# Kernel optimization log

Measured on AMD Instinct MI355X. Metric: run time of the kernel, lower is better.

Reference implementation:

```python
import jax, jax.numpy as jnp
import numpy as np

D = 768      # hidden_dim
H = 12       # num_heads
DH = D // H  # head_dim = 64
L = 12       # num_layers
V = 50257    # vocab_size
M = 16       # mini_batch_size (TTT chunk)
LR = 1.0     # ttt_learning_rate
EPS = 1e-5
ROPE_BASE = 10000.0


def _ln(x, w, b):
    mu = jnp.mean(x, axis=-1, keepdims=True)
    var = jnp.mean((x - mu) ** 2, axis=-1, keepdims=True)
    return (x - mu) / jnp.sqrt(var + EPS) * w + b


def _rope(x):
    # x: (B, H, S, DH)
    S, dh = x.shape[2], x.shape[3]
    half = dh // 2
    freqs = 1.0 / (ROPE_BASE ** (jnp.arange(half, dtype=x.dtype) / half))
    ang = jnp.arange(S, dtype=x.dtype)[:, None] * freqs[None, :]  # (S, half)
    cos, sin = jnp.cos(ang), jnp.sin(ang)
    x1, x2 = x[..., :half], x[..., half:]
    return jnp.concatenate([x1 * cos - x2 * sin, x1 * sin + x2 * cos], axis=-1)


def setup_inputs() -> dict:
    key = jax.random.key(0)
    ks = jax.random.split(key, 12)
    std = 0.02
    B, S = 4, 1024
    inp = {
        "input_ids": jax.random.randint(ks[0], (B, S), 0, V),
        "tok_emb": jax.random.normal(ks[1], (V, D), jnp.float32) * std,
        "emb_ln_w": jnp.ones((D,), jnp.float32),
        "emb_ln_b": jnp.zeros((D,), jnp.float32),
        "wq": jax.random.normal(ks[2], (L, D, D), jnp.float32) * std,
        "wk": jax.random.normal(ks[3], (L, D, D), jnp.float32) * std,
        "wv": jax.random.normal(ks[4], (L, D, D), jnp.float32) * std,
        "wo": jax.random.normal(ks[5], (L, D, D), jnp.float32) * std,
        "n1w": jnp.ones((L, D), jnp.float32),
        "n1b": jnp.zeros((L, D), jnp.float32),
        "n2w": jnp.ones((L, D), jnp.float32),
        "n2b": jnp.zeros((L, D), jnp.float32),
        "m1w": jax.random.normal(ks[6], (L, D, 4 * D), jnp.float32) * std,
        "m1b": jnp.zeros((L, 4 * D), jnp.float32),
        "m2w": jax.random.normal(ks[7], (L, 4 * D, D), jnp.float32) * std,
        "m2b": jnp.zeros((L, D), jnp.float32),
        "onw": jnp.ones((D,), jnp.float32),
        "onb": jnp.zeros((D,), jnp.float32),
    }
    return inp


def _forward(input_ids, tok_emb, emb_ln_w, emb_ln_b, wq, wk, wv, wo,
             n1w, n1b, n2w, n2b, m1w, m1b, m2w, m2b, onw, onb):
    B, S = input_ids.shape
    nc = S // M
    eta = LR / M
    mask = jnp.tril(jnp.ones((M, M), tok_emb.dtype))

    x = tok_emb[input_ids]                      # (B, S, D) token embedding
    x = _ln(x, emb_ln_w, emb_ln_b)

    def layer(x, p):
        (lwq, lwk, lwv, lwo, ln1w, ln1b, ln2w, ln2b,
         lm1w, lm1b, lm2w, lm2b) = p
        h = _ln(x, ln1w, ln1b)

        def proj(w):
            return (h @ w).reshape(B, S, H, DH).transpose(0, 2, 1, 3)  # (B,H,S,DH)

        q, k, v = proj(lwq), proj(lwk), proj(lwv)
        q, k = _rope(q), _rope(k)

        def chunks(t):  # (B,H,S,DH) -> (nc,B,H,M,DH)
            return t.reshape(B, H, nc, M, DH).transpose(2, 0, 1, 3, 4)

        qc, kc, vc = chunks(q), chunks(k), chunks(v)
        W0 = jnp.zeros((B, H, DH, DH), x.dtype)  # fast-weight state per head

        def step(W, c):
            qm, km, vm = c                                   # (B,H,M,DH)
            # reconstruction error of current fast weights on this chunk
            E = jnp.einsum('bhmd,bhde->bhme', km, W) - vm    # (B,H,M,DH)
            # causal intra-chunk correction (dual form of per-token GD)
            A = jnp.einsum('bhmd,bhnd->bhmn', qm, km) * mask
            O = (jnp.einsum('bhmd,bhde->bhme', qm, W)
                 - eta * jnp.einsum('bhmn,bhne->bhme', A, E))
            Wn = W - eta * jnp.einsum('bhmd,bhme->bhde', km, E)
            return Wn, O

        _, O = jax.lax.scan(step, W0, (qc, kc, vc))          # (nc,B,H,M,DH)
        o = O.transpose(1, 2, 0, 3, 4).reshape(B, H, S, DH)
        o = o.transpose(0, 2, 1, 3).reshape(B, S, D)
        x = x + o @ lwo

        h2 = _ln(x, ln2w, ln2b)
        x = x + jax.nn.gelu(h2 @ lm1w + lm1b) @ lm2w + lm2b
        return x, None

    x, _ = jax.lax.scan(layer, x,
                        (wq, wk, wv, wo, n1w, n1b, n2w, n2b,
                         m1w, m1b, m2w, m2b))
    x = _ln(x, onw, onb)
    logits = x @ tok_emb.T                                    # tied LM head
    return logits


def reference(input_ids, tok_emb, emb_ln_w, emb_ln_b, wq, wk, wv, wo,
              n1w, n1b, n2w, n2b, m1w, m1b, m2w, m2b, onw, onb):
    return _forward(input_ids, tok_emb, emb_ln_w, emb_ln_b, wq, wk, wv, wo,
                    n1w, n1b, n2w, n2b, m1w, m1b, m2w, m2b, onw, onb)
```

## Files before the change

### kernel.cpp

```cpp
#include <hip/hip_runtime.h>
#include <cstdint>
#include <cstddef>

#define Dm 768
#define Hh 12
#define DHd 64
#define Ll 12
#define Vv 50257
#define Vp 50304
#define Tt 4096
#define Ff 3072
#define QS 2304
#define ETA (1.0f/16.0f)

typedef __attribute__((ext_vector_type(8))) _Float16 half8;
typedef __attribute__((ext_vector_type(8))) unsigned short ushort8;
typedef __attribute__((ext_vector_type(4))) float f32x4;

static __device__ __forceinline__ unsigned short f2h(float f){
  union { _Float16 h; unsigned short u; } c; c.h = (_Float16)f; return c.u;
}
static __device__ __forceinline__ float h2f(unsigned short u){
  union { unsigned short u; _Float16 h; } c; c.u = u; return (float)c.h;
}
static __device__ __forceinline__ float4 h4(ushort4 u){
  float4 f; f.x=h2f(u.x); f.y=h2f(u.y); f.z=h2f(u.z); f.w=h2f(u.w); return f;
}
static __device__ __forceinline__ void gload16(const void* g, void* l){
  __builtin_amdgcn_global_load_lds((const __attribute__((address_space(1))) unsigned int*)g,
                                   (__attribute__((address_space(3))) unsigned int*)l, 16, 0, 0);
}
static __device__ __forceinline__ size_t pan_off(int ks, size_t M, int row, int k){
  return ((size_t)ks*M + row)*128 + (size_t)(((k*2) ^ ((row & 7) << 4)));
}

__global__ __launch_bounds__(256)
void convwt_kernel(const float* __restrict__ src, unsigned short* __restrict__ dst,
                   int K, int Ns, int Nd, int coff)
{
  const int l  = blockIdx.y;
  const int nb = blockIdx.x % (Ns/64);
  const int ks = blockIdx.x / (Ns/64);
  const int t  = threadIdx.x;
  __shared__ float tile[64][65];
  const float* W = src + (size_t)l*K*Ns;
  {
    const int r = t >> 2, c0 = (t & 3) * 16;
    const float* s = W + (size_t)(ks*64 + r)*Ns + nb*64 + c0;
    #pragma unroll
    for (int i = 0; i < 4; ++i) {
      const float4 f = *(const float4*)(s + i*4);
      tile[r][c0+i*4+0]=f.x; tile[r][c0+i*4+1]=f.y; tile[r][c0+i*4+2]=f.z; tile[r][c0+i*4+3]=f.w;
    }
  }
  __syncthreads();
  const int n   = t >> 2;
  const int kk0 = (t & 3) * 16;
  const int gn  = coff + nb*64 + n;
  unsigned short bh[16];
  #pragma unroll
  for (int i = 0; i < 16; ++i) bh[i] = f2h(tile[kk0 + i][n]);
  const size_t rowb = ((size_t)l*K*Nd + ((size_t)ks*Nd + gn)*64) * 2;
  const int swz = (gn & 7) << 4;
  char* bD = (char*)dst + rowb;
  *(ushort8*)(bD + ((kk0*2)      ^ swz)) = *(ushort8*)&bh[0];
  *(ushort8*)(bD + ((kk0*2 + 16) ^ swz)) = *(ushort8*)&bh[8];
}

__global__ __launch_bounds__(256)
void convtok_kernel(const float* __restrict__ src, unsigned short* __restrict__ dst)
{
  const int total = 12 * Vp * 8;
  for (int gi = blockIdx.x*256 + threadIdx.x; gi < total; gi += gridDim.x*256) {
    const int j  = gi & 7;
    const int v  = (gi >> 3) % Vp;
    const int ks = gi / (8 * Vp);
    ushort8 u;
    if (v < Vv) {
      const float* s = src + (size_t)v*Dm + ks*64 + j*8;
      const float4 f0 = *(const float4*)s, f1 = *(const float4*)(s+4);
      u[0]=f2h(f0.x); u[1]=f2h(f0.y); u[2]=f2h(f0.z); u[3]=f2h(f0.w);
      u[4]=f2h(f1.x); u[5]=f2h(f1.y); u[6]=f2h(f1.z); u[7]=f2h(f1.w);
    } else {
      #pragma unroll
      for (int q = 0; q < 8; ++q) u[q] = 0;
    }
    const size_t rowb = ((size_t)ks*Vp + v) * 128;
    *(ushort8*)((char*)dst + rowb + ((j*16) ^ ((v&7)<<4))) = u;
  }
}

__global__ __launch_bounds__(256)
void rtab_kernel(float* __restrict__ rt)
{
  const int idx = blockIdx.x*256 + threadIdx.x;
  if (idx >= 1024*64) return;
  const int s = idx >> 6, c = idx & 63, d = c & 31;
  const float freq = powf(10000.0f, -(float)d * (1.0f/32.0f));
  const float ang  = (float)s * freq;
  rt[idx] = (c < 32) ? cosf(ang) : sinf(ang);
}

template<int OMODE>
__global__ __launch_bounds__(256)
void ln_kernel(const float* __restrict__ in, const int* __restrict__ ids,
               const float* __restrict__ w, const float* __restrict__ b,
               void* __restrict__ o1)
{
  const int row = blockIdx.x;
  const int t = threadIdx.x;
  const float* px = in + (ids ? (size_t)ids[row] * Dm : (size_t)row * Dm);
  float x0 = px[t], x1 = px[t+256], x2 = px[t+512];
  float s  = x0 + x1 + x2;
  float s2 = x0*x0 + x1*x1 + x2*x2;
  #pragma unroll
  for (int o = 32; o > 0; o >>= 1) { s += __shfl_xor(s, o); s2 += __shfl_xor(s2, o); }
  __shared__ float ls[4], ls2[4];
  if ((t & 63) == 0) { ls[t>>6] = s; ls2[t>>6] = s2; }
  __syncthreads();
  s  = ls[0]+ls[1]+ls[2]+ls[3];
  s2 = ls2[0]+ls2[1]+ls2[2]+ls2[3];
  const float mu  = s * (1.0f/Dm);
  const float var = s2 * (1.0f/Dm) - mu*mu;
  const float rs  = rsqrtf(var + 1e-5f);
  #pragma unroll
  for (int i = 0; i < 3; ++i) {
    const int c = t + i*256;
    const float xv = (i==0) ? x0 : (i==1) ? x1 : x2;
    const float vv_ = (xv-mu)*rs*w[c] + b[c];
    if (OMODE == 0) {
      ((float*)o1)[(size_t)row * Dm + c] = vv_;
    } else {
      *(unsigned short*)((char*)o1 + pan_off(c >> 6, Tt, row, c & 63)) = f2h(vv_);
    }
  }
}

static __device__ __forceinline__ float4 rot4(float4 a, float4 p, float4 rc, float4 rs, bool hi){
  float4 o;
  if (hi) { o.x = p.x*rs.x + a.x*rc.x; o.y = p.y*rs.y + a.y*rc.y;
            o.z = p.z*rs.z + a.z*rc.z; o.w = p.w*rs.w + a.w*rc.w; }
  else    { o.x = a.x*rc.x - p.x*rs.x; o.y = a.y*rc.y - p.y*rs.y;
            o.z = a.z*rc.z - p.z*rs.z; o.w = a.w*rc.w - p.w*rs.w; }
  return o;
}

__global__ __launch_bounds__(256)
void ttt_scan_kernel(const unsigned short* __restrict__ qkv, const float* __restrict__ rt,
                     unsigned short* __restrict__ ob)
{
  const int head = blockIdx.x >> 2;
  const int es   = blockIdx.x & 3;
  const int b  = head / Hh;
  const int hd = head % Hh;
  const int t  = threadIdx.x;
  __shared__ float Wm[16][68];
  __shared__ float kms[16][68];
  __shared__ float qms[16][68];
  __shared__ float EsT[16][20];
  __shared__ float Asc[16][20];

  const int e   = t & 15;
  const int m16 = t >> 4;
  const int sr  = t >> 4;
  const int sc  = (t & 15) * 4;
  const bool hi = (sc >= 32);

  for (int i = t; i < 16*68; i += 256) ((float*)Wm)[i] = 0.0f;

  const int tb0 = b * 1024;
  const size_t gbase = (size_t)hd * DHd;

  float4 krR, qrR;
  {
    const size_t ro = (size_t)(tb0 + sr)*QS + gbase;
    const float4 kr = h4(*(const ushort4*)&qkv[ro + Dm + sc]);
    const float4 kp = h4(*(const ushort4*)&qkv[ro + Dm + (sc^32)]);
    const float4 qr = h4(*(const ushort4*)&qkv[ro + sc]);
    const float4 qp = h4(*(const ushort4*)&qkv[ro + (sc^32)]);
    const float4 rc = *(const float4*)&rt[sr*64 + (sc&31)];
    const float4 rs = *(const float4*)&rt[sr*64 + 32 + (sc&31)];
    krR = rot4(kr, kp, rc, rs, hi);
    qrR = rot4(qr, qp, rc, rs, hi);
  }
  __syncthreads();

  for (int c = 0; c < 64; ++c) {
    const int tb = tb0 + c*16;
    *(float4*)&kms[sr][sc] = krR;
    *(float4*)&qms[sr][sc] = qrR;
    __syncthreads();
    if (c < 63) {
      const size_t ro = (size_t)(tb + 16 + sr)*QS + gbase;
      const float4 kr = h4(*(const ushort4*)&qkv[ro + Dm + sc]);
      const float4 kp = h4(*(const ushort4*)&qkv[ro + Dm + (sc^32)]);
      const float4 qr = h4(*(const ushort4*)&qkv[ro + sc]);
      const float4 qp = h4(*(const ushort4*)&qkv[ro + (sc^32)]);
      const int sN = (c+1)*16 + sr;
      const float4 rc = *(const float4*)&rt[sN*64 + (sc&31)];
      const float4 rs = *(const float4*)&rt[sN*64 + 32 + (sc&31)];
      krR = rot4(kr, kp, rc, rs, hi);
      qrR = rot4(qr, qp, rc, rs, hi);
    }
    const float vreg = h2f(qkv[(size_t)(tb+m16)*QS + 2*Dm + gbase + es*16 + e]);
    float aE = -vreg, aO = 0.0f, aA = 0.0f;
    #pragma unroll
    for (int d4 = 0; d4 < 64; d4 += 4) {
      const float4 wv = *(const float4*)&Wm[e][d4];
      const float4 km = *(const float4*)&kms[m16][d4];
      const float4 qm = *(const float4*)&qms[m16][d4];
      const float4 ke = *(const float4*)&kms[e][d4];
      aE += km.x*wv.x + km.y*wv.y + km.z*wv.z + km.w*wv.w;
      aO += qm.x*wv.x + qm.y*wv.y + qm.z*wv.z + qm.w*wv.w;
      aA += qm.x*ke.x + qm.y*ke.y + qm.z*ke.z + qm.w*ke.w;
    }
    EsT[e][m16] = aE;
    Asc[m16][e] = (e <= m16) ? (-ETA * aA) : 0.0f;
    __syncthreads();
    float esr[16];
    float acc = aO;
    #pragma unroll
    for (int n4 = 0; n4 < 16; n4 += 4) {
      const float4 ev = *(const float4*)&EsT[e][n4];
      const float4 av = *(const float4*)&Asc[m16][n4];
      esr[n4]=ev.x; esr[n4+1]=ev.y; esr[n4+2]=ev.z; esr[n4+3]=ev.w;
      acc += av.x*ev.x + av.y*ev.y + av.z*ev.z + av.w*ev.w;
    }
    *(unsigned short*)((char*)ob + pan_off(hd, Tt, tb + m16, es*16 + e)) = f2h(acc);
    {
      const int d0 = m16 * 4;
      float4 wacc; wacc.x = 0.0f; wacc.y = 0.0f; wacc.z = 0.0f; wacc.w = 0.0f;
      #pragma unroll
      for (int m = 0; m < 16; ++m) {
        const float4 km = *(const float4*)&kms[m][d0];
        const float ev = esr[m];
        wacc.x += km.x*ev; wacc.y += km.y*ev; wacc.z += km.z*ev; wacc.w += km.w*ev;
      }
      float4 wv = *(float4*)&Wm[e][d0];
      wv.x -= ETA*wacc.x; wv.y -= ETA*wacc.y; wv.z -= ETA*wacc.z; wv.w -= ETA*wacc.w;
      *(float4*)&Wm[e][d0] = wv;
    }
    __syncthreads();
  }
}

static __device__ __forceinline__ float gelu_f(float x){
  const float u = 0.7978845608028654f * (x + 0.044715f * x*x*x);
  return 0.5f * x * (1.0f + tanhf(u));
}

template<int TM, int TN, int KP, bool BIAS, bool GELU_, bool RES, int OUT>
__global__ __launch_bounds__(256)
void gemm_kernel(const unsigned short* __restrict__ A, const unsigned short* __restrict__ B,
                 const float* __restrict__ bias, const float* __restrict__ res,
                 void* __restrict__ o1, int M, int N, int K)
{
  constexpr int FM = TM / 32;
  constexpr int FN = TN / 32;
  __shared__ __attribute__((aligned(16))) unsigned short As[KP*TM*64];
  __shared__ __attribute__((aligned(16))) unsigned short Bs[KP*TN*64];
  const int t    = threadIdx.x;
  const int lane = t & 63;
  const int fr   = lane & 15;
  const int fg   = lane >> 4;
  const int wave = t >> 6;
  const int wm   = (wave >> 1) * (TM/2);
  const int wn   = (wave & 1) * (TN/2);
  const int row0 = blockIdx.y * TM;
  const int n0   = blockIdx.x * TN;

  f32x4 acc[FM][FN];
  #pragma unroll
  for (int i = 0; i < FM; ++i)
    #pragma unroll
    for (int j = 0; j < FN; ++j)
      #pragma unroll
      for (int r = 0; r < 4; ++r) acc[i][j][r] = 0.0f;

  const int NI = K / (64*KP);
  for (int it = 0; it < NI; ++it) {
    #pragma unroll
    for (int p = 0; p < KP; ++p) {
      const int ks = it*KP + p;
      {
        const char* gB = (const char*)B + ((size_t)ks*N + n0) * 128;
        char* lB = (char*)Bs + p*(TN*128);
        #pragma unroll
        for (int r = 0; r < TN/32; ++r) {
          const int chunk = (r*4 + wave) * 1024;
          gload16(gB + chunk + lane*16, lB + chunk);
        }
      }
      {
        const char* gA = (const char*)A + ((size_t)ks*M + row0) * 128;
        char* lA = (char*)As + p*(TM*128);
        #pragma unroll
        for (int r = 0; r < TM/32; ++r) {
          const int chunk = (r*4 + wave) * 1024;
          gload16(gA + chunk + lane*16, lA + chunk);
        }
      }
    }
    __syncthreads();
    #pragma unroll
    for (int p = 0; p < KP; ++p) {
      #pragma unroll
      for (int kh = 0; kh < 2; ++kh) {
        half8 af[FM], bf[FN];
        const int swz = (fr & 7) << 4;
        #pragma unroll
        for (int mt = 0; mt < FM; ++mt)
          af[mt] = *(const half8*)((const char*)As + p*(TM*128) + (((wm + mt*16 + fr)*128 + kh*64 + fg*16) ^ swz));
        #pragma unroll
        for (int nt = 0; nt < FN; ++nt)
          bf[nt] = *(const half8*)((const char*)Bs + p*(TN*128) + (((wn + nt*16 + fr)*128 + kh*64 + fg*16) ^ swz));
        #pragma unroll
        for (int mt = 0; mt < FM; ++mt)
          #pragma unroll
          for (int nt = 0; nt < FN; ++nt)
            acc[mt][nt] = __builtin_amdgcn_mfma_f32_16x16x32_f16(af[mt], bf[nt], acc[mt][nt], 0, 0, 0);
      }
    }
    __syncthreads();
  }

  #pragma unroll
  for (int mt = 0; mt < FM; ++mt) {
    #pragma unroll
    for (int nt = 0; nt < FN; ++nt) {
      const int col = n0 + wn + nt*16 + fr;
      const int rbase = row0 + wm + mt*16 + fg*4;
      const float bcol = BIAS ? bias[col] : 0.0f;
      #pragma unroll
      for (int r = 0; r < 4; ++r) {
        float val = acc[mt][nt][r];
        if (BIAS)  val += bcol;
        if (GELU_) val = gelu_f(val);
        if (OUT == 1) {
          *(unsigned short*)((char*)o1 + pan_off(col >> 6, M, rbase + r, col & 63)) = f2h(val);
        } else if (OUT == 2) {
          ((unsigned short*)o1)[(size_t)(rbase + r) * N + col] = f2h(val);
        } else {
          const size_t off = (size_t)(rbase + r) * N + col;
          float v2 = val;
          if (RES) v2 += res[off];
          ((float*)o1)[off] = v2;
        }
      }
    }
  }
}

template<bool PRE>
__global__ __launch_bounds__(256)
void logits_kernel(const unsigned short* __restrict__ hop, const float* __restrict__ tok,
                   const unsigned short* __restrict__ tokb, float* __restrict__ C)
{
  __shared__ __attribute__((aligned(16))) unsigned short As[128*64];
  __shared__ __attribute__((aligned(16))) unsigned short Bs[128*64];
  int bid = blockIdx.x;
  bid = (bid & 7) * 1572 + (bid >> 3);
  const int n0   = (bid >> 5) * 128;
  const int row0 = (bid & 31) * 128;

  const int t    = threadIdx.x;
  const int lane = t & 63;
  const int fr   = lane & 15;
  const int fg   = lane >> 4;
  const int wave = t >> 6;
  const int wm   = (wave >> 1) * 64;
  const int wn   = (wave & 1) * 64;
  const int arow = t >> 1;
  const int ach  = (t & 1) * 32;

  f32x4 acc[4][4];
  #pragma unroll
  for (int i = 0; i < 4; ++i)
    #pragma unroll
    for (int j = 0; j < 4; ++j)
      #pragma unroll
      for (int r = 0; r < 4; ++r) acc[i][j][r] = 0.0f;

  for (int ks = 0; ks < 12; ++ks) {
    {
      const char* gA = (const char*)hop + ((size_t)ks*Tt + row0) * 128;
      #pragma unroll
      for (int p = 0; p < 4; ++p) {
        const int off = p*4096 + t*16;
        const ushort8 u = *(const ushort8*)(gA + off);
        *(ushort8*)((char*)As + off) = u;
      }
    }
    if (PRE) {
      const char* gB = (const char*)tokb + ((size_t)ks*Vp + n0) * 128;
      #pragma unroll
      for (int p = 0; p < 4; ++p) {
        const int off = p*4096 + t*16;
        const ushort8 u = *(const ushort8*)(gB + off);
        *(ushort8*)((char*)Bs + off) = u;
      }
    } else {
      const int brow = n0 + arow;
      if (brow < Vv) {
        const float* src = &tok[(size_t)brow * Dm + ks*64 + ach];
        #pragma unroll
        for (int i = 0; i < 4; ++i) {
          const float4 f0 = *(const float4*)(src + i*8);
          const float4 f1 = *(const float4*)(src + i*8 + 4);
          ushort8 u;
          u[0]=f2h(f0.x); u[1]=f2h(f0.y); u[2]=f2h(f0.z); u[3]=f2h(f0.w);
          u[4]=f2h(f1.x); u[5]=f2h(f1.y); u[6]=f2h(f1.z); u[7]=f2h(f1.w);
          const int byt = (arow*128 + (ach + i*8)*2) ^ ((arow & 7) << 4);
          *(ushort8*)((char*)Bs + byt) = u;
        }
      } else {
        ushort8 z;
        #pragma unroll
        for (int j = 0; j < 8; ++j) z[j] = 0;
        #pragma unroll
        for (int i = 0; i < 4; ++i) {
          const int byt = (arow*128 + (ach + i*8)*2) ^ ((arow & 7) << 4);
          *(ushort8*)((char*)Bs + byt) = z;
        }
      }
    }
    __syncthreads();
    #pragma unroll
    for (int kh = 0; kh < 2; ++kh) {
      half8 af[4], bf[4];
      const int swz = (fr & 7) << 4;
      #pragma unroll
      for (int mt = 0; mt < 4; ++mt)
        af[mt] = *(const half8*)((const char*)As + (((wm + mt*16 + fr)*128 + kh*64 + fg*16) ^ swz));
      #pragma unroll
      for (int nt = 0; nt < 4; ++nt)
        bf[nt] = *(const half8*)((const char*)Bs + (((wn + nt*16 + fr)*128 + kh*64 + fg*16) ^ swz));
      #pragma unroll
      for (int mt = 0; mt < 4; ++mt)
        #pragma unroll
        for (int nt = 0; nt < 4; ++nt)
          acc[mt][nt] = __builtin_amdgcn_mfma_f32_16x16x32_f16(af[mt], bf[nt], acc[mt][nt], 0, 0, 0);
    }
    __syncthreads();
  }

  #pragma unroll
  for (int mt = 0; mt < 4; ++mt) {
    #pragma unroll
    for (int nt = 0; nt < 4; ++nt) {
      const int col = n0 + wn + nt*16 + fr;
      if (col < Vv) {
        const int rbase = row0 + wm + mt*16 + fg*4;
        #pragma unroll
        for (int r = 0; r < 4; ++r)
          C[(size_t)(rbase + r) * Vv + col] = acc[mt][nt][r];
      }
    }
  }
}

extern "C" void kernel_launch(void* const* d_in, const int* in_sizes, int n_in,
                              void* d_out, int out_size, void* d_ws, size_t ws_size,
                              hipStream_t stream)
{
  const int*   ids = (const int*)  d_in[0];
  const float* tok = (const float*)d_in[1];
  const float* ew  = (const float*)d_in[2];
  const float* eb  = (const float*)d_in[3];
  const float* wq  = (const float*)d_in[4];
  const float* wk  = (const float*)d_in[5];
  const float* wv  = (const float*)d_in[6];
  const float* wo  = (const float*)d_in[7];
  const float* n1w = (const float*)d_in[8];
  const float* n1b = (const float*)d_in[9];
  const float* n2w = (const float*)d_in[10];
  const float* n2b = (const float*)d_in[11];
  const float* m1w = (const float*)d_in[12];
  const float* m1b = (const float*)d_in[13];
  const float* m2w = (const float*)d_in[14];
  const float* m2b = (const float*)d_in[15];
  const float* onw = (const float*)d_in[16];
  const float* onb = (const float*)d_in[17];

  const size_t SP = (size_t)12 * Tt * 64;
  float* x = (float*)d_ws;
  unsigned short* hP = (unsigned short*)(x + (size_t)Tt * Dm);
  unsigned short* ho = hP + SP;
  float* rt = (float*)(ho + SP);
  unsigned short* tokb = (unsigned short*)(rt + 1024*64);
  const size_t ws_need = (size_t)Tt*Dm*4 + SP*2*2 + 1024*64*4 + (size_t)12*Vp*64*2;
  const bool pre = (ws_size >= ws_need);

  float* out = (float*)d_out;
  unsigned short* gP  = (unsigned short*)d_out;
  unsigned short* qkv = (unsigned short*)((char*)d_out + (size_t)28*1024*1024);
  unsigned short* obP = (unsigned short*)((char*)d_out + (size_t)50*1024*1024);
  unsigned short* wbase = (unsigned short*)((char*)d_out + (size_t)60*1024*1024);
  const size_t SQKV = (size_t)Ll * Dm * QS;
  const size_t SWO  = (size_t)Ll * Dm * Dm;
  const size_t SM   = (size_t)Ll * Dm * Ff;
  unsigned short* qkvW = wbase;
  unsigned short* woW  = qkvW + SQKV;
  unsigned short* m1W  = woW  + SWO;
  unsigned short* m2W  = m1W  + SM;

  convwt_kernel<<<dim3(12*12, Ll), 256, 0, stream>>>(wq, qkvW, Dm, Dm, QS, 0);
  convwt_kernel<<<dim3(12*12, Ll), 256, 0, stream>>>(wk, qkvW, Dm, Dm, QS, Dm);
  convwt_kernel<<<dim3(12*12, Ll), 256, 0, stream>>>(wv, qkvW, Dm, Dm, QS, 2*Dm);
  convwt_kernel<<<dim3(12*12, Ll), 256, 0, stream>>>(wo, woW, Dm, Dm, Dm, 0);
  convwt_kernel<<<dim3(12*48, Ll), 256, 0, stream>>>(m1w, m1W, Dm, Ff, Ff, 0);
  convwt_kernel<<<dim3(48*12, Ll), 256, 0, stream>>>(m2w, m2W, Ff, Dm, Dm, 0);
  rtab_kernel<<<256, 256, 0, stream>>>(rt);
  if (pre) convtok_kernel<<<2048, 256, 0, stream>>>(tok, tokb);

  ln_kernel<0><<<Tt, 256, 0, stream>>>(tok, ids, ew, eb, x);

  for (int l = 0; l < Ll; ++l) {
    ln_kernel<1><<<Tt, 256, 0, stream>>>(x, nullptr, n1w + l*Dm, n1b + l*Dm, hP);
    gemm_kernel<128,128,1,false,false,false,2><<<dim3(QS/128, Tt/128), 256, 0, stream>>>(
        hP, qkvW + (size_t)l*Dm*QS, nullptr, nullptr, qkv, Tt, QS, Dm);
    ttt_scan_kernel<<<192, 256, 0, stream>>>(qkv, rt, obP);
    gemm_kernel<64,64,2,false,false,true,0><<<dim3(Dm/64, Tt/64), 256, 0, stream>>>(
        obP, woW + (size_t)l*Dm*Dm, nullptr, x, x, Tt, Dm, Dm);
    ln_kernel<1><<<Tt, 256, 0, stream>>>(x, nullptr, n2w + l*Dm, n2b + l*Dm, hP);
    gemm_kernel<128,128,1,true,true,false,1><<<dim3(Ff/128, Tt/128), 256, 0, stream>>>(
        hP, m1W + (size_t)l*Dm*Ff, m1b + (size_t)l*Ff, nullptr, gP, Tt, Ff, Dm);
    gemm_kernel<64,64,2,true,false,true,0><<<dim3(Dm/64, Tt/64), 256, 0, stream>>>(
        gP, m2W + (size_t)l*Ff*Dm, m2b + (size_t)l*Dm, x, x, Tt, Dm, Ff);
  }

  ln_kernel<1><<<Tt, 256, 0, stream>>>(x, nullptr, onw, onb, ho);
  if (pre)
    logits_kernel<true><<<dim3(12576, 1), 256, 0, stream>>>(ho, tok, tokb, out);
  else
    logits_kernel<false><<<dim3(12576, 1), 256, 0, stream>>>(ho, tok, nullptr, out);
}
```

Baseline: 4.165 ms.

## Enlarge logits tile to 256 rows with 512 threads and direct-to-LDS loads

Reworks the LM-head logits GEMM so each block covers 256 token rows by 128 vocab columns using 8 waves, which halves the number of times each vocab tile is loaded and converted. The A and B tiles now come in through a gload16 helper that writes straight into LDS instead of staging in registers. The wave-to-row mapping and the fp32-to-fp16 B conversion are rearranged for the new thread count. The larger LDS footprint and 512-thread blocks may lower occupancy, and the asynchronous loads depend on the gload16 helper's semantics and synchronisation being correct.

New measurement: 3.990 ms. 1.04x faster.

```diff
diff --git a/kernel.cpp b/kernel.cpp
--- a/kernel.cpp
+++ b/kernel.cpp
@@ -352,26 +352,26 @@
 }
 
 template<bool PRE>
-__global__ __launch_bounds__(256)
+__global__ __launch_bounds__(512)
 void logits_kernel(const unsigned short* __restrict__ hop, const float* __restrict__ tok,
                    const unsigned short* __restrict__ tokb, float* __restrict__ C)
 {
-  __shared__ __attribute__((aligned(16))) unsigned short As[128*64];
+  __shared__ __attribute__((aligned(16))) unsigned short As[256*64];
   __shared__ __attribute__((aligned(16))) unsigned short Bs[128*64];
   int bid = blockIdx.x;
-  bid = (bid & 7) * 1572 + (bid >> 3);
-  const int n0   = (bid >> 5) * 128;
-  const int row0 = (bid & 31) * 128;
+  bid = (bid & 7) * 786 + (bid >> 3);
+  const int n0   = (bid >> 4) * 128;
+  const int row0 = (bid & 15) * 256;
 
   const int t    = threadIdx.x;
   const int lane = t & 63;
   const int fr   = lane & 15;
   const int fg   = lane >> 4;
-  const int wave = t >> 6;
-  const int wm   = (wave >> 1) * 64;
-  const int wn   = (wave & 1) * 64;
-  const int arow = t >> 1;
-  const int ach  = (t & 1) * 32;
+  const int w    = t >> 6;
+  const int wm   = (w >> 1) * 64;
+  const int wn   = (w & 1) * 64;
+  const int arow = t >> 2;
+  const int ach  = (t & 3) * 16;
 
   f32x4 acc[4][4];
   #pragma unroll
@@ -385,43 +385,42 @@
     {
       const char* gA = (const char*)hop + ((size_t)ks*Tt + row0) * 128;
       #pragma unroll
-      for (int p = 0; p < 4; ++p) {
-        const int off = p*4096 + t*16;
-        const ushort8 u = *(const ushort8*)(gA + off);
-        *(ushort8*)((char*)As + off) = u;
+      for (int r = 0; r < 4; ++r) {
+        const int chunk = (r*8 + w) * 1024;
+        gload16(gA + chunk + lane*16, (char*)As + chunk);
       }
     }
     if (PRE) {
       const char* gB = (const char*)tokb + ((size_t)ks*Vp + n0) * 128;
       #pragma unroll
-      for (int p = 0; p < 4; ++p) {
-        const int off = p*4096 + t*16;
-        const ushort8 u = *(const ushort8*)(gB + off);
-        *(ushort8*)((char*)Bs + off) = u;
+      for (int r = 0; r < 2; ++r) {
+        const int chunk = (r*8 + w) * 1024;
+        gload16(gB + chunk + lane*16, (char*)Bs + chunk);
       }
     } else {
       const int brow = n0 + arow;
+      ushort8 u;
       if (brow < Vv) {
         const float* src = &tok[(size_t)brow * Dm + ks*64 + ach];
-        #pragma unroll
-        for (int i = 0; i < 4; ++i) {
-          const float4 f0 = *(const float4*)(src + i*8);
-          const float4 f1 = *(const float4*)(src + i*8 + 4);
-          ushort8 u;
-          u[0]=f2h(f0.x); u[1]=f2h(f0.y); u[2]=f2h(f0.z); u[3]=f2h(f0.w);
-          u[4]=f2h(f1.x); u[5]=f2h(f1.y); u[6]=f2h(f1.z); u[7]=f2h(f1.w);
-          const int byt = (arow*128 + (ach + i*8)*2) ^ ((arow & 7) << 4);
-          *(ushort8*)((char*)Bs + byt) = u;
-        }
+        const float4 f0 = *(const float4*)src;
+        const float4 f1 = *(const float4*)(src + 4);
+        const float4 f2 = *(const float4*)(src + 8);
+        const float4 f3 = *(const float4*)(src + 12);
+        u[0]=f2h(f0.x); u[1]=f2h(f0.y); u[2]=f2h(f0.z); u[3]=f2h(f0.w);
+        u[4]=f2h(f1.x); u[5]=f2h(f1.y); u[6]=f2h(f1.z); u[7]=f2h(f1.w);
+        const int byt0 = (arow*128 + ach*2) ^ ((arow & 7) << 4);
+        *(ushort8*)((char*)Bs + byt0) = u;
+        u[0]=f2h(f2.x); u[1]=f2h(f2.y); u[2]=f2h(f2.z); u[3]=f2h(f2.w);
+        u[4]=f2h(f3.x); u[5]=f2h(f3.y); u[6]=f2h(f3.z); u[7]=f2h(f3.w);
+        const int byt1 = (arow*128 + ach*2 + 16) ^ ((arow & 7) << 4);
+        *(ushort8*)((char*)Bs + byt1) = u;
       } else {
-        ushort8 z;
-        #pragma unroll
-        for (int j = 0; j < 8; ++j) z[j] = 0;
-        #pragma unroll
-        for (int i = 0; i < 4; ++i) {
-          const int byt = (arow*128 + (ach + i*8)*2) ^ ((arow & 7) << 4);
-          *(ushort8*)((char*)Bs + byt) = z;
-        }
+        #pragma unroll
+        for (int q = 0; q < 8; ++q) u[q] = 0;
+        const int byt0 = (arow*128 + ach*2) ^ ((arow & 7) << 4);
+        const int byt1 = (arow*128 + ach*2 + 16) ^ ((arow & 7) << 4);
+        *(ushort8*)((char*)Bs + byt0) = u;
+        *(ushort8*)((char*)Bs + byt1) = u;
       }
     }
     __syncthreads();
@@ -450,7 +449,7 @@
     for (int nt = 0; nt < 4; ++nt) {
       const int col = n0 + wn + nt*16 + fr;
       if (col < Vv) {
-        const int rbase = row0 + wm + mt*16 + fg*4;
+        const int rbase = row0 + wm*0 + (w >> 1)*64 + mt*16 + fg*4;
         #pragma unroll
         for (int r = 0; r < 4; ++r)
           C[(size_t)(rbase + r) * Vv + col] = acc[mt][nt][r];
@@ -531,7 +530,7 @@
 
   ln_kernel<1><<<Tt, 256, 0, stream>>>(x, nullptr, onw, onb, ho);
   if (pre)
-    logits_kernel<true><<<dim3(12576, 1), 256, 0, stream>>>(ho, tok, tokb, out);
+    logits_kernel<true><<<dim3(6288, 1), 512, 0, stream>>>(ho, tok, tokb, out);
   else
-    logits_kernel<false><<<dim3(12576, 1), 256, 0, stream>>>(ho, tok, nullptr, out);
-}
+    logits_kernel<false><<<dim3(6288, 1), 512, 0, stream>>>(ho, tok, nullptr, out);
+}
```
